# Performance work log

Hardware: AMD Instinct MI355X
Metric: run time of the kernel (lower is better)

Reference implementation:

```python
import jax, jax.numpy as jnp
import numpy as np

B_, T_, IN_, OUT_, N_ = 16, 4096, 512, 512, 512


def setup_inputs() -> dict:
    key = jax.random.key(0)
    ks = jax.random.split(key, 9)
    u = jax.random.normal(ks[0], (B_, T_, IN_), dtype=jnp.float32)
    # LRU init per original module
    rmin, rmax, max_phase = 0.9, 1.0, 6.283
    u1 = jax.random.uniform(ks[1], (N_,), dtype=jnp.float32)
    u2 = jax.random.uniform(ks[2], (N_,), dtype=jnp.float32)
    nu_log = jnp.log(-0.5 * jnp.log(u1 * (rmax + rmin) * (rmax - rmin) + rmin ** 2))
    theta_log = jnp.log(max_phase * u2)
    Lambda_mod = jnp.exp(-jnp.exp(nu_log))
    gamma_log = jnp.log(jnp.sqrt(1.0 - jnp.square(Lambda_mod)))
    B_re = jax.random.normal(ks[3], (N_, IN_), dtype=jnp.float32) / np.sqrt(2 * IN_)
    B_im = jax.random.normal(ks[4], (N_, IN_), dtype=jnp.float32) / np.sqrt(2 * IN_)
    C_re = jax.random.normal(ks[5], (OUT_, N_), dtype=jnp.float32) / np.sqrt(N_)
    C_im = jax.random.normal(ks[6], (OUT_, N_), dtype=jnp.float32) / np.sqrt(N_)
    D = jax.random.normal(ks[7], (OUT_, IN_), dtype=jnp.float32) / np.sqrt(IN_)
    return {"u": u, "nu_log": nu_log, "theta_log": theta_log, "gamma_log": gamma_log,
            "B_re": B_re, "B_im": B_im, "C_re": C_re, "C_im": C_im, "D": D}


def reference(u, nu_log, theta_log, gamma_log, B_re, B_im, C_re, C_im, D):
    # Lambda: diagonal complex transition, |Lambda| = exp(-exp(nu_log)), angle = exp(theta_log)
    mod = jnp.exp(-jnp.exp(nu_log))             # [N]
    theta = jnp.exp(theta_log)
    Lam = jax.lax.complex(mod * jnp.cos(theta), mod * jnp.sin(theta))  # [N] complex64
    gammas = jnp.exp(gamma_log)                  # [N]
    Bc = jax.lax.complex(B_re, B_im) * gammas[:, None]                 # [N, IN]
    Cc = jax.lax.complex(C_re, C_im)                                   # [OUT, N]

    # input projection: Bu[b,t,n] = sum_i Bc[n,i] * u[b,t,i]
    Bu = jnp.einsum('bti,ni->btn', u.astype(Bc.dtype), Bc)             # [B,T,N] complex

    # diagonal linear recurrence x_t = Lam * x_{t-1} + Bu_t, state starts at 0
    a = jnp.broadcast_to(Lam, Bu.shape)

    def combine(e1, e2):
        a1, b1 = e1
        a2, b2 = e2
        return a1 * a2, a2 * b1 + b2

    _, x = jax.lax.associative_scan(combine, (a, Bu), axis=1)          # x: [B,T,N]

    y = 2.0 * jnp.einsum('btn,on->bto', x, Cc).real + jnp.einsum('bti,oi->bto', u, D)
    return y
```

## Files before the change

### kernel.cpp

```cpp
#include <hip/hip_runtime.h>
#include <hip/hip_bf16.h>
#include <cstdint>
#include <cstddef>


using short8 = __attribute__((ext_vector_type(8))) short;
using f32x4 = __attribute__((ext_vector_type(4))) float;

#define BDIM 16
#define TDIM 4096
#define MTOT (BDIM * TDIM)
#define CHUNK 64
#define NCHUNK (TDIM / CHUNK)

__device__ __forceinline__ unsigned short f2bf(float f) {
    unsigned u = __float_as_uint(f);
    u = u + 0x7FFFu + ((u >> 16) & 1u);
    return (unsigned short)(u >> 16);
}
__device__ __forceinline__ float bflo(unsigned w) { return __uint_as_float(w << 16); }
__device__ __forceinline__ float bfhi(unsigned w) { return __uint_as_float(w & 0xFFFF0000u); }

__device__ __forceinline__ size_t perm_off(int row, int kt, int kp, int rowbytes) {
    int kk = kp >> 5, km = kp & 31;
    int half = km >> 4;
    int g = (km & 15) >> 2, j = km & 3;
    int cc = (kk << 2) | g;
    int c = cc ^ (row & 7);
    return (size_t)row * rowbytes + kt * 128 + (c << 4) + half * 8 + j * 2;
}

__device__ __forceinline__ void gload_lds16(const void* g, void* l) {
    __builtin_amdgcn_global_load_lds((const __attribute__((address_space(1))) void*)g,
                                     (__attribute__((address_space(3))) void*)l, 16, 0, 0);
}

__global__ void prep_w1(const float* __restrict__ B_re, const float* __restrict__ B_im,
                        const float* __restrict__ gamma_log, char* __restrict__ W1) {
    int i = blockIdx.x * 256 + threadIdx.x;
    int r = blockIdx.y;
    int n = r >> 1;
    float gmm = expf(gamma_log[n]);
    float v = (r & 1) ? B_im[n * 512 + i] * gmm : B_re[n * 512 + i] * gmm;
    *(unsigned short*)(W1 + perm_off(r, i >> 6, i & 63, 1024)) = f2bf(v);
}

__global__ void prep_w2(const float* __restrict__ C_re, const float* __restrict__ C_im,
                        const float* __restrict__ D, char* __restrict__ W2) {
    int k = blockIdx.x * 256 + threadIdx.x;
    int o = blockIdx.y;
    float v;
    if (k < 1024) {
        int n = k >> 1;
        v = (k & 1) ? -2.0f * C_im[o * 512 + n] : 2.0f * C_re[o * 512 + n];
    } else {
        v = D[o * 512 + (k - 1024)];
    }
    *(unsigned short*)(W2 + perm_off(o, k >> 6, k & 63, 3072)) = f2bf(v);
}

__global__ void convert_u(const float4* __restrict__ u4, char* __restrict__ Apack) {
    size_t idx = (size_t)blockIdx.x * 256 + threadIdx.x;
    float4 v = u4[idx];
    int row = (int)(idx >> 7);
    int c4 = (int)(idx & 127);
    int kg = 1024 + c4 * 4;
    unsigned lo = (unsigned)f2bf(v.x) | ((unsigned)f2bf(v.y) << 16);
    unsigned hi = (unsigned)f2bf(v.z) | ((unsigned)f2bf(v.w) << 16);
    size_t off = perm_off(row, kg >> 6, kg & 63, 3072);
    *reinterpret_cast<uint2*>(Apack + off) = make_uint2(lo, hi);
}

template <int OUT_MODE, int NBN>
__global__ __launch_bounds__(256) void gemm_nt(const char* __restrict__ A, int ldab,
                                               const char* __restrict__ Bm, int ldbb,
                                               void* __restrict__ Cout, int ktiles) {
    __shared__ __align__(16) char As[128 * 128];
    __shared__ __align__(16) char Bs[128 * 128];
    const int tid = threadIdx.x;
    const int lane = tid & 63, w = tid >> 6;
    const int bid = blockIdx.x;
    const int cpx = gridDim.x >> 3;
    const int swz = (bid & 7) * cpx + (bid >> 3);
    const int bm = swz / NBN, bn = swz % NBN;
    const int wm = (w >> 1) * 64, wn = (w & 1) * 64;
    const int ml = lane & 15, g = lane >> 4;

    const int srow = w * 32 + (lane >> 3);
    const int schunk = lane & 7;
    const char* Ag = A + (size_t)(bm * 128 + srow) * ldab + schunk * 16;
    const char* Bg = Bm + (size_t)(bn * 128 + srow) * ldbb + schunk * 16;
    char* AsW = &As[w * 4096];
    char* BsW = &Bs[w * 4096];

    f32x4 acc[4][4] = {};

    for (int kt = 0; kt < ktiles; ++kt) {
#pragma unroll
        for (int p = 0; p < 4; ++p) {
            gload_lds16(Ag + (size_t)p * 8 * ldab + kt * 128, AsW + p * 1024);
            gload_lds16(Bg + (size_t)p * 8 * ldbb + kt * 128, BsW + p * 1024);
        }
        __syncthreads();
#pragma unroll
        for (int kk = 0; kk < 2; ++kk) {
            short8 af[4], bfr[4];
#pragma unroll
            for (int mt = 0; mt < 4; ++mt) {
                int r = wm + mt * 16 + ml;
                af[mt] = *reinterpret_cast<const short8*>(
                    As + r * 128 + ((((kk << 2) | g) ^ (r & 7)) << 4));
            }
#pragma unroll
            for (int nt = 0; nt < 4; ++nt) {
                int r = wn + nt * 16 + ml;
                bfr[nt] = *reinterpret_cast<const short8*>(
                    Bs + r * 128 + ((((kk << 2) | g) ^ (r & 7)) << 4));
            }
#pragma unroll
            for (int mt = 0; mt < 4; ++mt)
#pragma unroll
                for (int nt = 0; nt < 4; ++nt)
                    acc[mt][nt] = __builtin_amdgcn_mfma_f32_16x16x32_bf16(af[mt], bfr[nt], acc[mt][nt], 0, 0, 0);
        }
        __syncthreads();
    }

#pragma unroll
    for (int mt = 0; mt < 4; ++mt) {
#pragma unroll
        for (int nt = 0; nt < 4; ++nt) {
#pragma unroll
            for (int r = 0; r < 4; ++r) {
                int grow = bm * 128 + wm + mt * 16 + g * 4 + r;
                int gcol = bn * 128 + wn + nt * 16 + ml;
                float v = acc[mt][nt][r];
                if (OUT_MODE == 0) {
                    reinterpret_cast<float*>(Cout)[(size_t)grow * 512 + gcol] = v;
                } else {
                    reinterpret_cast<unsigned short*>(Cout)[(size_t)grow * 1024 + gcol] = f2bf(v);
                }
            }
        }
    }
}

__global__ void scan_carry(const unsigned* __restrict__ Bu, const float* __restrict__ nu_log,
                           const float* __restrict__ theta_log, float2* __restrict__ carry) {
    int q = blockIdx.x * 256 + threadIdx.x;
    int n = q & 511, c = (q >> 9) & 63, b = q >> 15;
    float mod = expf(-expf(nu_log[n]));
    float th = expf(theta_log[n]);
    float s, co;
    sincosf(th, &s, &co);
    float Lre = mod * co, Lim = mod * s;
    const unsigned* p = Bu + ((size_t)(b * TDIM + c * CHUNK)) * 512 + n;
    float xr = 0.f, xi = 0.f;
#pragma unroll 8
    for (int t = 0; t < CHUNK; ++t) {
        unsigned wv = p[(size_t)t * 512];
        float nr = fmaf(Lre, xr, fmaf(-Lim, xi, bflo(wv)));
        float ni = fmaf(Lre, xi, fmaf(Lim, xr, bfhi(wv)));
        xr = nr; xi = ni;
    }
    carry[(size_t)(b * NCHUNK + c) * 512 + n] = make_float2(xr, xi);
}

__global__ void scan_prefix(const float2* __restrict__ carry, const float* __restrict__ nu_log,
                            const float* __restrict__ theta_log, float2* __restrict__ prefix) {
    int q = blockIdx.x * 256 + threadIdx.x;
    int n = q & 511, b = q >> 9;
    float e = expf(nu_log[n]);
    float modL = expf(-(float)CHUNK * e);
    float th = expf(theta_log[n]);
    double ang = fmod((double)CHUNK * (double)th, 6.283185307179586);
    float s, co;
    sincosf((float)ang, &s, &co);
    float Lre = modL * co, Lim = modL * s;
    float pr = 0.f, pi = 0.f;
    for (int c = 0; c < NCHUNK; ++c) {
        size_t idx = (size_t)(b * NCHUNK + c) * 512 + n;
        prefix[idx] = make_float2(pr, pi);
        float2 ev = carry[idx];
        float nr = fmaf(Lre, pr, fmaf(-Lim, pi, ev.x));
        float ni = fmaf(Lre, pi, fmaf(Lim, pr, ev.y));
        pr = nr; pi = ni;
    }
}

__global__ void scan_apply(const unsigned* __restrict__ Bu, const float* __restrict__ nu_log,
                           const float* __restrict__ theta_log, const float2* __restrict__ prefix,
                           char* __restrict__ Apack) {
    int q = blockIdx.x * 256 + threadIdx.x;
    int n = q & 511, c = (q >> 9) & 63, b = q >> 15;
    float mod = expf(-expf(nu_log[n]));
    float th = expf(theta_log[n]);
    float s, co;
    sincosf(th, &s, &co);
    float Lre = mod * co, Lim = mod * s;
    const unsigned* p = Bu + ((size_t)(b * TDIM + c * CHUNK)) * 512 + n;
    float2 pv = prefix[(size_t)(b * NCHUNK + c) * 512 + n];
    float xr = pv.x, xi = pv.y;
    int kp = (2 * n) & 63;
    int kk = kp >> 5, km = kp & 31;
    int half = km >> 4, gg = (km & 15) >> 2, j = km & 3;
    int cc = (kk << 2) | gg;
    int partial = (n >> 5) * 128 + half * 8 + j * 2;
    int row0 = b * TDIM + c * CHUNK;
#pragma unroll 8
    for (int t = 0; t < CHUNK; ++t) {
        unsigned wv = p[(size_t)t * 512];
        float nr = fmaf(Lre, xr, fmaf(-Lim, xi, bflo(wv)));
        float ni = fmaf(Lre, xi, fmaf(Lim, xr, bfhi(wv)));
        xr = nr; xi = ni;
        int row = row0 + t;
        size_t off = (size_t)row * 3072 + ((cc ^ (row & 7)) << 4) + partial;
        *reinterpret_cast<unsigned*>(Apack + off) =
            (unsigned)f2bf(xr) | ((unsigned)f2bf(xi) << 16);
    }
}

extern "C" void kernel_launch(void* const* d_in, const int* in_sizes, int n_in,
                              void* d_out, int out_size, void* d_ws, size_t ws_size,
                              hipStream_t stream) {
    const float* u         = (const float*)d_in[0];
    const float* nu_log    = (const float*)d_in[1];
    const float* theta_log = (const float*)d_in[2];
    const float* gamma_log = (const float*)d_in[3];
    const float* B_re      = (const float*)d_in[4];
    const float* B_im      = (const float*)d_in[5];
    const float* C_re      = (const float*)d_in[6];
    const float* C_im      = (const float*)d_in[7];
    const float* D         = (const float*)d_in[8];

    char* ws = (char*)d_ws;
    char* Apack = ws;
    size_t off = (size_t)MTOT * 3072;
    char* W1 = ws + off; off += 1024 * 1024;
    char* W2 = ws + off; off += 512 * 3072;
    float2* carry  = (float2*)(ws + off); off += (size_t)BDIM * NCHUNK * 512 * 8;
    float2* prefix = (float2*)(ws + off); off += (size_t)BDIM * NCHUNK * 512 * 8;

    unsigned short* Bu = (unsigned short*)d_out;

    prep_w1<<<dim3(2, 1024), 256, 0, stream>>>(B_re, B_im, gamma_log, W1);
    prep_w2<<<dim3(6, 512), 256, 0, stream>>>(C_re, C_im, D, W2);
    convert_u<<<32768, 256, 0, stream>>>((const float4*)u, Apack);
    gemm_nt<1, 8><<<4096, 256, 0, stream>>>(Apack + 16 * 128, 3072, W1, 1024, (void*)Bu, 8);
    scan_carry<<<2048, 256, 0, stream>>>((const unsigned*)Bu, nu_log, theta_log, carry);
    scan_prefix<<<32, 256, 0, stream>>>(carry, nu_log, theta_log, prefix);
    scan_apply<<<2048, 256, 0, stream>>>((const unsigned*)Bu, nu_log, theta_log, prefix, Apack);
    gemm_nt<0, 4><<<2048, 256, 0, stream>>>(Apack, 3072, W2, 3072, d_out, 24);
}
```

Measured before the change: 365.5 us.

## Enlarge GEMM tiles to 256x256, double-buffer LDS, fuse chunk-carry scan into GEMM

The bf16 MFMA GEMM moves to 512-thread blocks computing 256x256 tiles. It double-buffers LDS with explicit vmcnt waits so the next k-tile's loads overlap the MFMAs, and raises wave priority during the MFMA sequence. The first GEMM stages its bf16 Bu tile in LDS and computes the per-chunk scan carries in its epilogue, which removes the separate scan_carry kernel and its re-read of Bu. In exchange it uses 128KB of LDS and many more accumulator registers, which may lower occupancy. The mapping from tile to channel and chunk in the fused carry (nglob = bn*128 + n_local) looks suspicious for 256-wide tiles that hold interleaved re/im columns.

```diff
diff --git a/kernel.cpp b/kernel.cpp
--- a/kernel.cpp
+++ b/kernel.cpp
@@ -71,42 +71,58 @@
     *reinterpret_cast<uint2*>(Apack + off) = make_uint2(lo, hi);
 }
 
+#define ASM_VMCNT8 asm volatile("s_waitcnt vmcnt(8)" ::: "memory")
+#define ASM_VMCNT0 asm volatile("s_waitcnt vmcnt(0)" ::: "memory")
+#define ASM_LGKM0  asm volatile("s_waitcnt lgkmcnt(0)" ::: "memory")
+
 template <int OUT_MODE, int NBN>
-__global__ __launch_bounds__(256) void gemm_nt(const char* __restrict__ A, int ldab,
-                                               const char* __restrict__ Bm, int ldbb,
-                                               void* __restrict__ Cout, int ktiles) {
-    __shared__ __align__(16) char As[128 * 128];
-    __shared__ __align__(16) char Bs[128 * 128];
+__global__ __launch_bounds__(512, 2) void gemm_nt(const char* __restrict__ A, int ldab,
+                                                  const char* __restrict__ Bm, int ldbb,
+                                                  void* __restrict__ Cout, int ktiles,
+                                                  float2* __restrict__ carry,
+                                                  const float* __restrict__ nu_log,
+                                                  const float* __restrict__ theta_log) {
+    __shared__ __align__(16) char lds[131072];
     const int tid = threadIdx.x;
     const int lane = tid & 63, w = tid >> 6;
     const int bid = blockIdx.x;
     const int cpx = gridDim.x >> 3;
     const int swz = (bid & 7) * cpx + (bid >> 3);
     const int bm = swz / NBN, bn = swz % NBN;
-    const int wm = (w >> 1) * 64, wn = (w & 1) * 64;
+    const int wm = (w >> 2) * 128, wn = (w & 3) * 64;
     const int ml = lane & 15, g = lane >> 4;
 
-    const int srow = w * 32 + (lane >> 3);
-    const int schunk = lane & 7;
-    const char* Ag = A + (size_t)(bm * 128 + srow) * ldab + schunk * 16;
-    const char* Bg = Bm + (size_t)(bn * 128 + srow) * ldbb + schunk * 16;
-    char* AsW = &As[w * 4096];
-    char* BsW = &Bs[w * 4096];
-
-    f32x4 acc[4][4] = {};
+    const char* Agr = A + (size_t)(bm * 256 + w * 32 + (lane >> 3)) * ldab + (lane & 7) * 16;
+    const char* Bgr = Bm + (size_t)(bn * 256 + w * 32 + (lane & 63 ? (lane >> 3) : 0)) * ldbb + (lane & 7) * 16;
+    const char* Bgr2 = Bm + (size_t)(bn * 256 + w * 32 + (lane >> 3)) * ldbb + (lane & 7) * 16;
+
+#define STAGE(q, kt_) do {                                                            \
+        _Pragma("unroll")                                                             \
+        for (int p = 0; p < 4; ++p) {                                                 \
+            gload_lds16(Agr + (size_t)(p * 8) * ldab + (size_t)(kt_) * 128,           \
+                        lds + (q) * 65536 + w * 4096 + p * 1024);                     \
+            gload_lds16(Bgr2 + (size_t)(p * 8) * ldbb + (size_t)(kt_) * 128,          \
+                        lds + (q) * 65536 + 32768 + w * 4096 + p * 1024);             \
+        }                                                                             \
+    } while (0)
+
+    f32x4 acc[8][4] = {};
+
+    STAGE(0, 0);
+    STAGE(1, 1);
 
     for (int kt = 0; kt < ktiles; ++kt) {
-#pragma unroll
-        for (int p = 0; p < 4; ++p) {
-            gload_lds16(Ag + (size_t)p * 8 * ldab + kt * 128, AsW + p * 1024);
-            gload_lds16(Bg + (size_t)p * 8 * ldbb + kt * 128, BsW + p * 1024);
-        }
-        __syncthreads();
+        const int cur = kt & 1;
+        if (kt + 2 <= ktiles) { ASM_VMCNT8; } else { ASM_VMCNT0; }
+        __builtin_amdgcn_s_barrier();
+        __builtin_amdgcn_sched_barrier(0);
+        const char* As = lds + cur * 65536;
+        const char* Bs = lds + cur * 65536 + 32768;
 #pragma unroll
         for (int kk = 0; kk < 2; ++kk) {
-            short8 af[4], bfr[4];
-#pragma unroll
-            for (int mt = 0; mt < 4; ++mt) {
+            short8 af[8], bfr[4];
+#pragma unroll
+            for (int mt = 0; mt < 8; ++mt) {
                 int r = wm + mt * 16 + ml;
                 af[mt] = *reinterpret_cast<const short8*>(
                     As + r * 128 + ((((kk << 2) | g) ^ (r & 7)) << 4));
@@ -117,53 +133,69 @@
                 bfr[nt] = *reinterpret_cast<const short8*>(
                     Bs + r * 128 + ((((kk << 2) | g) ^ (r & 7)) << 4));
             }
-#pragma unroll
-            for (int mt = 0; mt < 4; ++mt)
+            __builtin_amdgcn_s_setprio(1);
+#pragma unroll
+            for (int mt = 0; mt < 8; ++mt)
 #pragma unroll
                 for (int nt = 0; nt < 4; ++nt)
                     acc[mt][nt] = __builtin_amdgcn_mfma_f32_16x16x32_bf16(af[mt], bfr[nt], acc[mt][nt], 0, 0, 0);
+            __builtin_amdgcn_s_setprio(0);
         }
-        __syncthreads();
-    }
-
-#pragma unroll
-    for (int mt = 0; mt < 4; ++mt) {
-#pragma unroll
-        for (int nt = 0; nt < 4; ++nt) {
-#pragma unroll
-            for (int r = 0; r < 4; ++r) {
-                int grow = bm * 128 + wm + mt * 16 + g * 4 + r;
-                int gcol = bn * 128 + wn + nt * 16 + ml;
-                float v = acc[mt][nt][r];
-                if (OUT_MODE == 0) {
-                    reinterpret_cast<float*>(Cout)[(size_t)grow * 512 + gcol] = v;
-                } else {
-                    reinterpret_cast<unsigned short*>(Cout)[(size_t)grow * 1024 + gcol] = f2bf(v);
+        ASM_LGKM0;
+        __builtin_amdgcn_s_barrier();
+        if (kt + 2 < ktiles) STAGE(cur, kt + 2);
+    }
+
+    if (OUT_MODE == 0) {
+        float* O = (float*)Cout;
+#pragma unroll
+        for (int mt = 0; mt < 8; ++mt)
+#pragma unroll
+            for (int nt = 0; nt < 4; ++nt)
+#pragma unroll
+                for (int r_ = 0; r_ < 4; ++r_) {
+                    int grow = bm * 256 + wm + mt * 16 + g * 4 + r_;
+                    int gcol = bn * 256 + wn + nt * 16 + ml;
+                    O[(size_t)grow * 512 + gcol] = acc[mt][nt][r_];
                 }
-            }
+    } else {
+        unsigned short* BuOut = (unsigned short*)Cout;
+#pragma unroll
+        for (int mt = 0; mt < 8; ++mt)
+#pragma unroll
+            for (int nt = 0; nt < 4; ++nt)
+#pragma unroll
+                for (int r_ = 0; r_ < 4; ++r_) {
+                    int lrow = wm + mt * 16 + g * 4 + r_;
+                    int lcol = wn + nt * 16 + ml;
+                    unsigned short hv = f2bf(acc[mt][nt][r_]);
+                    *(unsigned short*)(lds + lrow * 512 + lcol * 2) = hv;
+                    BuOut[(size_t)(bm * 256 + lrow) * 1024 + bn * 256 + lcol] = hv;
+                }
+        ASM_LGKM0;
+        __builtin_amdgcn_s_barrier();
+        __builtin_amdgcn_sched_barrier(0);
+        int n_local = tid & 127, c_local = tid >> 7;
+        int nglob = bn * 128 + n_local;
+        float mod = expf(-expf(nu_log[nglob]));
+        float th = expf(theta_log[nglob]);
+        float s, co;
+        sincosf(th, &s, &co);
+        float Lre = mod * co, Lim = mod * s;
+        const char* base = lds + (c_local * 64) * 512 + n_local * 4;
+        float xr = 0.f, xi = 0.f;
+#pragma unroll 8
+        for (int t = 0; t < 64; ++t) {
+            unsigned wv = *reinterpret_cast<const unsigned*>(base + t * 512);
+            float nr = fmaf(Lre, xr, fmaf(-Lim, xi, bflo(wv)));
+            float ni = fmaf(Lre, xi, fmaf(Lim, xr, bfhi(wv)));
+            xr = nr; xi = ni;
         }
-    }
-}
-
-__global__ void scan_carry(const unsigned* __restrict__ Bu, const float* __restrict__ nu_log,
-                           const float* __restrict__ theta_log, float2* __restrict__ carry) {
-    int q = blockIdx.x * 256 + threadIdx.x;
-    int n = q & 511, c = (q >> 9) & 63, b = q >> 15;
-    float mod = expf(-expf(nu_log[n]));
-    float th = expf(theta_log[n]);
-    float s, co;
-    sincosf(th, &s, &co);
-    float Lre = mod * co, Lim = mod * s;
-    const unsigned* p = Bu + ((size_t)(b * TDIM + c * CHUNK)) * 512 + n;
-    float xr = 0.f, xi = 0.f;
-#pragma unroll 8
-    for (int t = 0; t < CHUNK; ++t) {
-        unsigned wv = p[(size_t)t * 512];
-        float nr = fmaf(Lre, xr, fmaf(-Lim, xi, bflo(wv)));
-        float ni = fmaf(Lre, xi, fmaf(Lim, xr, bfhi(wv)));
-        xr = nr; xi = ni;
-    }
-    carry[(size_t)(b * NCHUNK + c) * 512 + n] = make_float2(xr, xi);
+        int b = (bm * 256) >> 12;
+        int cglob = (((bm * 256) & 4095) >> 6) + c_local;
+        carry[(size_t)(b * NCHUNK + cglob) * 512 + nglob] = make_float2(xr, xi);
+    }
+#undef STAGE
 }
 
 __global__ void scan_prefix(const float2* __restrict__ carry, const float* __restrict__ nu_log,
@@ -246,9 +278,10 @@
     prep_w1<<<dim3(2, 1024), 256, 0, stream>>>(B_re, B_im, gamma_log, W1);
     prep_w2<<<dim3(6, 512), 256, 0, stream>>>(C_re, C_im, D, W2);
     convert_u<<<32768, 256, 0, stream>>>((const float4*)u, Apack);
-    gemm_nt<1, 8><<<4096, 256, 0, stream>>>(Apack + 16 * 128, 3072, W1, 1024, (void*)Bu, 8);
-    scan_carry<<<2048, 256, 0, stream>>>((const unsigned*)Bu, nu_log, theta_log, carry);
+    gemm_nt<1, 4><<<1024, 512, 0, stream>>>(Apack + 16 * 128, 3072, W1, 1024,
+                                            (void*)Bu, 8, carry, nu_log, theta_log);
     scan_prefix<<<32, 256, 0, stream>>>(carry, nu_log, theta_log, prefix);
     scan_apply<<<2048, 256, 0, stream>>>((const unsigned*)Bu, nu_log, theta_log, prefix, Apack);
-    gemm_nt<0, 4><<<2048, 256, 0, stream>>>(Apack, 3072, W2, 3072, d_out, 24);
-}
+    gemm_nt<0, 2><<<512, 512, 0, stream>>>(Apack, 3072, W2, 3072, d_out, 24,
+                                           nullptr, nullptr, nullptr);
+}
```

Measured after the change: 320.2 us. 12.4% less time.
